# Optimization experiments

Hardware: AMD Instinct MI355X
Metric: run time of the kernel (lower is better)

Reference implementation:

```python
import jax, jax.numpy as jnp
import numpy as np

NUM_NODES = 100000
OUT_CHANNELS = 64
NUM_EDGES = 3200000


def setup_inputs() -> dict:
    key = jax.random.key(0)
    k1, k2, k3 = jax.random.split(key, 3)
    edge_index = jax.random.randint(k1, (2, NUM_EDGES), 0, NUM_NODES, dtype=jnp.int64) if jax.config.jax_enable_x64 else jax.random.randint(k1, (2, NUM_EDGES), 0, NUM_NODES, dtype=jnp.int32)
    # nn.Linear default init: U(-1/sqrt(fan_in), 1/sqrt(fan_in)); use randn-scale for a correctness baseline
    W_weight = jax.random.normal(k2, (OUT_CHANNELS, NUM_NODES), dtype=jnp.float32) * (1.0 / np.sqrt(NUM_NODES))
    W_bias = jax.random.normal(k3, (OUT_CHANNELS,), dtype=jnp.float32) * (1.0 / np.sqrt(NUM_NODES))
    return {"edge_index": edge_index, "W_weight": W_weight, "W_bias": W_bias}


def reference(edge_index, W_weight, W_bias):
    # A is the [N, N] binary COO adjacency (duplicate edges sum, matching
    # an uncoalesced torch sparse COO matmul). logits = A @ W_weight.T + b.
    num_nodes = W_weight.shape[1]
    row = edge_index[0] - jnp.min(edge_index[0])  # row = row - row.min()
    col = edge_index[1]
    Wt = W_weight.T  # [N, C]
    # SpMM as gather + segment-sum: logits[i] = sum_{(i,j) in E} Wt[j]
    logits = jax.ops.segment_sum(Wt[col], row, num_segments=num_nodes)  # [N, C]
    logits = logits + W_bias
    return jax.nn.log_softmax(logits, axis=1)
```

## Files before the change

kernel.cpp:

```cpp
#include <hip/hip_runtime.h>
#include <hip/hip_bf16.h>
#include <hip/hip_fp8.h>
#include <limits.h>

#define NUM_NODES 100000
#define OUT_CH 64
#define NUM_EDGES 3200000
#define BROWS 64
#define BSHIFT 6
#define NBUCK 1563
#define NBUCK_EXT 3125
#define NPBLK 128
#define EPB (NUM_EDGES / NPBLK)
#define I4PB (EPB / 4)
#define STAGECAP 4096
#define NTRANS 1563
#define FP8_SCALE 256.0f
#define FP8_INV (1.0f / 256.0f)

typedef float v2f __attribute__((ext_vector_type(2)));

__device__ __forceinline__ float fp8_decode_slow(unsigned b) {
    unsigned s = b >> 7, e = (b >> 3) & 0xF, m = b & 7;
    float v = (e == 0) ? ldexpf((float)m, -9) : ldexpf((float)(8 + m), (int)e - 10);
    return s ? -v : v;
}

__global__ __launch_bounds__(256) void LINK_62689342652831_mth_kernel(
    const float* __restrict__ W, unsigned char* __restrict__ Wt8,
    const int* __restrict__ rows, int* __restrict__ minp, int* __restrict__ hist2d) {
    __shared__ float tile[64][65];
    if (blockIdx.x < NTRANS) {
        int n0 = blockIdx.x * 64;
        int tx = threadIdx.x & 63;
        int ty = threadIdx.x >> 6;
        for (int c = ty; c < 64; c += 4) {
            int n = n0 + tx;
            tile[c][tx] = (n < NUM_NODES) ? W[(size_t)c * NUM_NODES + n] : 0.0f;
        }
        __syncthreads();
        for (int i = ty; i < 64; i += 4) {
            int n = n0 + i;
            if (n < NUM_NODES) {
                __hip_fp8_e4m3 q(FP8_SCALE * tile[tx][i]);
                Wt8[(size_t)n * OUT_CH + tx] = *reinterpret_cast<unsigned char*>(&q);
            }
        }
    } else {
        int blk = blockIdx.x - NTRANS;
        int* h = (int*)tile;
        int* sm = (int*)tile + 2048;
        for (int i = threadIdx.x; i < NBUCK; i += 256) h[i] = 0;
        __syncthreads();
        const int4* r4 = (const int4*)rows;
        int m = INT_MAX;
        for (int i = threadIdx.x; i < I4PB; i += 256) {
            int4 v = r4[blk * I4PB + i];
            m = min(m, min(min(v.x, v.y), min(v.z, v.w)));
            atomicAdd(&h[(unsigned)v.x >> BSHIFT], 1);
            atomicAdd(&h[(unsigned)v.y >> BSHIFT], 1);
            atomicAdd(&h[(unsigned)v.z >> BSHIFT], 1);
            atomicAdd(&h[(unsigned)v.w >> BSHIFT], 1);
        }
        for (int off = 32; off > 0; off >>= 1) m = min(m, __shfl_xor(m, off, 64));
        if ((threadIdx.x & 63) == 0) sm[threadIdx.x >> 6] = m;
        __syncthreads();
        for (int i = threadIdx.x; i < NBUCK; i += 256) hist2d[blk * NBUCK + i] = h[i];
        if (threadIdx.x == 0)
            atomicMin(minp, min(min(sm[0], sm[1]), min(sm[2], sm[3])));
    }
}

__global__ __launch_bounds__(512) void LINK_62689342652831_colscan_kernel(
    int* __restrict__ hist2d, int* __restrict__ totals) {
    int lane = threadIdx.x & 63;
    int wid = threadIdx.x >> 6;
    int b = blockIdx.x * 8 + wid;
    if (b >= NBUCK) return;
    int carry = 0;
    for (int rnd = 0; rnd < NPBLK / 64; ++rnd) {
        int blk = rnd * 64 + lane;
        int v = hist2d[blk * NBUCK + b];
        int x = v;
        for (int off = 1; off < 64; off <<= 1) {
            int y = __shfl_up(x, off, 64);
            if (lane >= off) x += y;
        }
        hist2d[blk * NBUCK + b] = x - v + carry;
        carry += __shfl(x, 63, 64);
    }
    if (lane == 0) totals[b] = carry;
}

__global__ __launch_bounds__(1024) void LINK_62689342652831_bscan_kernel(
    const int* __restrict__ totals, int* __restrict__ bstart) {
    __shared__ int ss[1024];
    int t = threadIdx.x;
    int i0 = 2 * t, i1 = 2 * t + 1;
    int v0 = (i0 < NBUCK) ? totals[i0] : 0;
    int v1 = (i1 < NBUCK) ? totals[i1] : 0;
    int p1 = v0 + v1;
    ss[t] = p1;
    __syncthreads();
    for (int off = 1; off < 1024; off <<= 1) {
        int x = (t >= off) ? ss[t - off] : 0;
        __syncthreads();
        ss[t] += x;
        __syncthreads();
    }
    int texcl = ss[t] - p1;
    if (i0 < NBUCK) bstart[i0] = texcl;
    if (i1 < NBUCK) bstart[i1] = texcl + v0;
    if (t == 1023) bstart[NBUCK] = ss[1023];
}

__global__ __launch_bounds__(512) void LINK_62689342652831_part_kernel(
    const int* __restrict__ rows, const int* __restrict__ cols,
    const int* __restrict__ hist2d, const int* __restrict__ bstart,
    unsigned int* __restrict__ packed) {
    __shared__ int offs_l[NBUCK];
    __shared__ int lcur[NBUCK];
    int blk = blockIdx.x;
    for (int i = threadIdx.x; i < NBUCK; i += 512) {
        offs_l[i] = bstart[i] + hist2d[blk * NBUCK + i];
        lcur[i] = 0;
    }
    __syncthreads();
    const int4* r4 = (const int4*)rows;
    const int4* c4 = (const int4*)cols;
    for (int i = threadIdx.x; i < I4PB; i += 512) {
        int4 rv = r4[blk * I4PB + i];
        int4 cv = c4[blk * I4PB + i];
#pragma unroll
        for (int k = 0; k < 4; ++k) {
            int r = (k == 0) ? rv.x : (k == 1) ? rv.y : (k == 2) ? rv.z : rv.w;
            int c = (k == 0) ? cv.x : (k == 1) ? cv.y : (k == 2) ? cv.z : cv.w;
            int b = (unsigned)r >> BSHIFT;
            int pos = offs_l[b] + atomicAdd(&lcur[b], 1);
            packed[pos] = ((unsigned)(r & (BROWS - 1)) << 17) | (unsigned)c;
        }
    }
}

__global__ __launch_bounds__(256) void LINK_62689342652831_spmm_kernel(
    const unsigned int* __restrict__ packed, const int* __restrict__ bstart,
    const unsigned char* __restrict__ Wt8, const float* __restrict__ bias,
    const int* __restrict__ minp, float* __restrict__ out) {
    __shared__ unsigned int sorted[STAGECAP];
    __shared__ int rhist[BROWS];
    __shared__ int rstart[BROWS + 1];
    __shared__ int rcur[BROWS];

    int lane = threadIdx.x & 63;
    int wid = threadIdx.x >> 6;
    int b = blockIdx.x;
    int minv = *minp;
    if (b * BROWS - minv >= NUM_NODES) return;
    int s = 0, e = 0;
    if (b < NBUCK) { s = bstart[b]; e = bstart[b + 1]; }
    int n = e - s;

    if (n <= STAGECAP) {
        int a4 = (4 - (s & 3)) & 3;
        if (a4 > n) a4 = n;
        int nb = (n - a4) >> 2;
        int tl = a4 + nb * 4;
        const uint4* p4 = (const uint4*)(packed + s + a4);

        if (threadIdx.x < BROWS) rhist[threadIdx.x] = 0;
        __syncthreads();
        if (threadIdx.x < a4) atomicAdd(&rhist[packed[s + threadIdx.x] >> 17], 1);
        for (int i = threadIdx.x; i < nb; i += 256) {
            uint4 u = p4[i];
            atomicAdd(&rhist[u.x >> 17], 1);
            atomicAdd(&rhist[u.y >> 17], 1);
            atomicAdd(&rhist[u.z >> 17], 1);
            atomicAdd(&rhist[u.w >> 17], 1);
        }
        if (tl + (int)threadIdx.x < n)
            atomicAdd(&rhist[packed[s + tl + threadIdx.x] >> 17], 1);
        __syncthreads();
        if (threadIdx.x < 64) {
            int c0 = rhist[lane];
            int x0 = c0;
            for (int off = 1; off < 64; off <<= 1) {
                int y0 = __shfl_up(x0, off, 64);
                if (lane >= off) x0 += y0;
            }
            rstart[lane] = x0 - c0;
            rcur[lane] = x0 - c0;
            if (lane == 63) rstart[64] = x0;
        }
        __syncthreads();
        if (threadIdx.x < a4) {
            unsigned int u = packed[s + threadIdx.x];
            sorted[atomicAdd(&rcur[u >> 17], 1)] = u;
        }
        for (int i = threadIdx.x; i < nb; i += 256) {
            uint4 u = p4[i];
            sorted[atomicAdd(&rcur[u.x >> 17], 1)] = u.x;
            sorted[atomicAdd(&rcur[u.y >> 17], 1)] = u.y;
            sorted[atomicAdd(&rcur[u.z >> 17], 1)] = u.z;
            sorted[atomicAdd(&rcur[u.w >> 17], 1)] = u.w;
        }
        if (tl + (int)threadIdx.x < n) {
            unsigned int u = packed[s + tl + threadIdx.x];
            sorted[atomicAdd(&rcur[u >> 17], 1)] = u;
        }
        __syncthreads();

        const unsigned int* Wt1 = (const unsigned int*)Wt8;
        int q = lane >> 4;
        int ql = lane & 15;
        float b0 = bias[4 * ql], b1 = bias[4 * ql + 1],
              b2 = bias[4 * ql + 2], b3 = bias[4 * ql + 3];

        for (int r = wid; r < BROWS; r += 4) {
            int gr = b * BROWS + r - minv;
            if (gr < 0 || gr >= NUM_NODES) continue;
            int s0 = rstart[r], e0 = rstart[r + 1];
            v2f a01 = {0.0f, 0.0f}, a23 = {0.0f, 0.0f};
            int i = s0 + q;
            for (; i + 4 < e0; i += 8) {
                unsigned int ua = sorted[i], ub = sorted[i + 4];
                unsigned int wa = Wt1[(size_t)((ua & 0x1FFFFu) << 4) + ql];
                unsigned int wb = Wt1[(size_t)((ub & 0x1FFFFu) << 4) + ql];
#if __has_builtin(__builtin_amdgcn_cvt_pk_f32_fp8)
                a01 += __builtin_amdgcn_cvt_pk_f32_fp8((int)wa, false);
                a23 += __builtin_amdgcn_cvt_pk_f32_fp8((int)wa, true);
                a01 += __builtin_amdgcn_cvt_pk_f32_fp8((int)wb, false);
                a23 += __builtin_amdgcn_cvt_pk_f32_fp8((int)wb, true);
#else
                a01.x += fp8_decode_slow(wa & 0xFF) + fp8_decode_slow(wb & 0xFF);
                a01.y += fp8_decode_slow((wa >> 8) & 0xFF) + fp8_decode_slow((wb >> 8) & 0xFF);
                a23.x += fp8_decode_slow((wa >> 16) & 0xFF) + fp8_decode_slow((wb >> 16) & 0xFF);
                a23.y += fp8_decode_slow(wa >> 24) + fp8_decode_slow(wb >> 24);
#endif
            }
            for (; i < e0; i += 4) {
                unsigned int w = Wt1[(size_t)((sorted[i] & 0x1FFFFu) << 4) + ql];
#if __has_builtin(__builtin_amdgcn_cvt_pk_f32_fp8)
                a01 += __builtin_amdgcn_cvt_pk_f32_fp8((int)w, false);
                a23 += __builtin_amdgcn_cvt_pk_f32_fp8((int)w, true);
#else
                a01.x += fp8_decode_slow(w & 0xFF);
                a01.y += fp8_decode_slow((w >> 8) & 0xFF);
                a23.x += fp8_decode_slow((w >> 16) & 0xFF);
                a23.y += fp8_decode_slow(w >> 24);
#endif
            }
            float a0 = a01.x, a1 = a01.y, a2 = a23.x, a3 = a23.y;
            a0 += __shfl_xor(a0, 32, 64); a1 += __shfl_xor(a1, 32, 64);
            a2 += __shfl_xor(a2, 32, 64); a3 += __shfl_xor(a3, 32, 64);
            a0 += __shfl_xor(a0, 16, 64); a1 += __shfl_xor(a1, 16, 64);
            a2 += __shfl_xor(a2, 16, 64); a3 += __shfl_xor(a3, 16, 64);

            float x0 = a0 * FP8_INV + b0, x1 = a1 * FP8_INV + b1;
            float x2 = a2 * FP8_INV + b2, x3 = a3 * FP8_INV + b3;
            float m = fmaxf(fmaxf(x0, x1), fmaxf(x2, x3));
            for (int off = 8; off > 0; off >>= 1) m = fmaxf(m, __shfl_xor(m, off, 64));
            float ssum = expf(x0 - m) + expf(x1 - m) + expf(x2 - m) + expf(x3 - m);
            for (int off = 8; off > 0; off >>= 1) ssum += __shfl_xor(ssum, off, 64);
            float l = m + logf(ssum);
            if (lane < 16) {
                float4 o = {x0 - l, x1 - l, x2 - l, x3 - l};
                *(float4*)&out[(size_t)gr * OUT_CH + 4 * ql] = o;
            }
        }
    } else {
        float* acc = (float*)sorted;
        for (int i = threadIdx.x; i < BROWS * OUT_CH; i += 256) acc[i] = 0.0f;
        __syncthreads();
        for (int i = s + wid; i < e; i += 4) {
            unsigned int u = packed[i];
            float v = fp8_decode_slow(Wt8[(size_t)(u & 0x1FFFF) * OUT_CH + lane]);
            atomicAdd(&acc[(u >> 17) * OUT_CH + lane], v);
        }
        __syncthreads();
        float bsv = bias[lane];
        for (int r = wid; r < BROWS; r += 4) {
            int gr = b * BROWS + r - minv;
            if (gr < 0 || gr >= NUM_NODES) continue;
            float x = acc[r * OUT_CH + lane] * FP8_INV + bsv;
            float m = x;
            for (int off = 32; off > 0; off >>= 1) m = fmaxf(m, __shfl_xor(m, off, 64));
            float ex = expf(x - m);
            float ssum = ex;
            for (int off = 32; off > 0; off >>= 1) ssum += __shfl_xor(ssum, off, 64);
            out[(size_t)gr * OUT_CH + lane] = x - m - logf(ssum);
        }
    }
}

__global__ void LINK_62689342652831_minf_kernel(const int* __restrict__ rows, int n,
                                                int* __restrict__ minp) {
    int tid = blockIdx.x * blockDim.x + threadIdx.x;
    int stride = gridDim.x * blockDim.x;
    int m = INT_MAX;
    for (int i = tid; i < n; i += stride) m = min(m, rows[i]);
    for (int off = 32; off > 0; off >>= 1) m = min(m, __shfl_xor(m, off, 64));
    if ((threadIdx.x & 63) == 0) atomicMin(minp, m);
}

__global__ void LINK_62689342652831_scatter_kernel(const int* __restrict__ rows,
                                                   const int* __restrict__ cols,
                                                   const float* __restrict__ W,
                                                   const int* __restrict__ minp,
                                                   float* __restrict__ out) {
    int lane = threadIdx.x & 63;
    int gw = (blockIdx.x * blockDim.x + threadIdx.x) >> 6;
    int nw = (gridDim.x * blockDim.x) >> 6;
    int minv = *minp;
    for (int e = gw; e < NUM_EDGES; e += nw) {
        int r = rows[e] - minv;
        int c = cols[e];
        float v = W[(size_t)lane * NUM_NODES + c];
        unsafeAtomicAdd(&out[(size_t)r * 64 + lane], v);
    }
}

__global__ void LINK_62689342652831_logsoftmax_kernel(float* __restrict__ out,
                                                      const float* __restrict__ bias) {
    int lane = threadIdx.x & 63;
    int gw = (blockIdx.x * blockDim.x + threadIdx.x) >> 6;
    int nw = (gridDim.x * blockDim.x) >> 6;
    float b = bias[lane];
    for (int r = gw; r < NUM_NODES; r += nw) {
        float x = out[(size_t)r * 64 + lane] + b;
        float m = x;
        for (int off = 32; off > 0; off >>= 1) m = fmaxf(m, __shfl_xor(m, off, 64));
        float e = expf(x - m);
        float s = e;
        for (int off = 32; off > 0; off >>= 1) s += __shfl_xor(s, off, 64);
        out[(size_t)r * 64 + lane] = x - m - logf(s);
    }
}

extern "C" void kernel_launch(void* const* d_in, const int* in_sizes, int n_in,
                              void* d_out, int out_size, void* d_ws, size_t ws_size,
                              hipStream_t stream) {
    const int* edges = (const int*)d_in[0];
    const int* rows = edges;
    const int* cols = edges + NUM_EDGES;
    const float* W = (const float*)d_in[1];
    const float* bias = (const float*)d_in[2];
    float* out = (float*)d_out;

    char* ws = (char*)d_ws;
    const size_t OFF_MIN = 0;
    const size_t OFF_TOT = 1024;
    const size_t OFF_BSTART = 16384;
    const size_t OFF_H2D = 32768;
    const size_t OFF_PACKED = 1024 * 1024;
    const size_t OFF_WT8 = OFF_PACKED + (size_t)NUM_EDGES * 4;
    const size_t need = OFF_WT8 + (size_t)NUM_NODES * OUT_CH;

    int* minp = (int*)(ws + OFF_MIN);
    int* totals = (int*)(ws + OFF_TOT);
    int* bstart = (int*)(ws + OFF_BSTART);
    int* hist2d = (int*)(ws + OFF_H2D);
    unsigned int* packed = (unsigned int*)(ws + OFF_PACKED);
    unsigned char* Wt8 = (unsigned char*)(ws + OFF_WT8);

    hipMemsetAsync(minp, 0x7f, sizeof(int), stream);

    if (ws_size >= need) {
        LINK_62689342652831_mth_kernel<<<NTRANS + NPBLK, 256, 0, stream>>>(W, Wt8, rows,
                                                                           minp, hist2d);
        LINK_62689342652831_colscan_kernel<<<(NBUCK + 7) / 8, 512, 0, stream>>>(hist2d, totals);
        LINK_62689342652831_bscan_kernel<<<1, 1024, 0, stream>>>(totals, bstart);
        LINK_62689342652831_part_kernel<<<NPBLK, 512, 0, stream>>>(rows, cols, hist2d,
                                                                   bstart, packed);
        LINK_62689342652831_spmm_kernel<<<NBUCK_EXT, 256, 0, stream>>>(packed, bstart, Wt8,
                                                                       bias, minp, out);
    } else {
        LINK_62689342652831_minf_kernel<<<2048, 256, 0, stream>>>(rows, NUM_EDGES, minp);
        hipMemsetAsync(d_out, 0, (size_t)out_size * sizeof(float), stream);
        LINK_62689342652831_scatter_kernel<<<2048, 256, 0, stream>>>(rows, cols, W, minp, out);
        LINK_62689342652831_logsoftmax_kernel<<<4096, 256, 0, stream>>>(out, bias);
    }
}
```

Measured before the change: 122.7 us.

## Fuse histogram and scan into partition kernel; gather per-block segments in SpMM

The separate histogram, column-scan and bucket-scan kernels are removed. Each partition block now builds its own local bucket histogram, scans it locally and scatters edges into its own slice of the packed array. The SpMM kernel reads the per-block segment offsets for its bucket, prefix-sums them and gathers edges from all 256 partition segments through a binary search into a shared staging buffer. This cuts two kernel launches and a global scan pass. In exchange the SpMM kernel does scattered, non-contiguous reads, a 256-way scan per block and more shared memory, and the transpose now runs serially before partitioning instead of alongside the histogram.

```diff
diff --git a/kernel.cpp b/kernel.cpp
--- a/kernel.cpp
+++ b/kernel.cpp
@@ -9,8 +9,9 @@
 #define BROWS 64
 #define BSHIFT 6
 #define NBUCK 1563
+#define NBUCKP (NBUCK + 1)
 #define NBUCK_EXT 3125
-#define NPBLK 128
+#define NPBLK 256
 #define EPB (NUM_EDGES / NPBLK)
 #define I4PB (EPB / 4)
 #define STAGECAP 4096
@@ -26,109 +27,89 @@
     return s ? -v : v;
 }
 
-__global__ __launch_bounds__(256) void LINK_62689342652831_mth_kernel(
-    const float* __restrict__ W, unsigned char* __restrict__ Wt8,
-    const int* __restrict__ rows, int* __restrict__ minp, int* __restrict__ hist2d) {
+__global__ __launch_bounds__(256) void LINK_62689342652831_transpose_kernel(
+    const float* __restrict__ W, unsigned char* __restrict__ Wt8) {
     __shared__ float tile[64][65];
-    if (blockIdx.x < NTRANS) {
-        int n0 = blockIdx.x * 64;
-        int tx = threadIdx.x & 63;
-        int ty = threadIdx.x >> 6;
-        for (int c = ty; c < 64; c += 4) {
-            int n = n0 + tx;
-            tile[c][tx] = (n < NUM_NODES) ? W[(size_t)c * NUM_NODES + n] : 0.0f;
-        }
-        __syncthreads();
-        for (int i = ty; i < 64; i += 4) {
-            int n = n0 + i;
-            if (n < NUM_NODES) {
-                __hip_fp8_e4m3 q(FP8_SCALE * tile[tx][i]);
-                Wt8[(size_t)n * OUT_CH + tx] = *reinterpret_cast<unsigned char*>(&q);
-            }
-        }
-    } else {
-        int blk = blockIdx.x - NTRANS;
-        int* h = (int*)tile;
-        int* sm = (int*)tile + 2048;
-        for (int i = threadIdx.x; i < NBUCK; i += 256) h[i] = 0;
-        __syncthreads();
-        const int4* r4 = (const int4*)rows;
-        int m = INT_MAX;
-        for (int i = threadIdx.x; i < I4PB; i += 256) {
-            int4 v = r4[blk * I4PB + i];
-            m = min(m, min(min(v.x, v.y), min(v.z, v.w)));
-            atomicAdd(&h[(unsigned)v.x >> BSHIFT], 1);
-            atomicAdd(&h[(unsigned)v.y >> BSHIFT], 1);
-            atomicAdd(&h[(unsigned)v.z >> BSHIFT], 1);
-            atomicAdd(&h[(unsigned)v.w >> BSHIFT], 1);
-        }
-        for (int off = 32; off > 0; off >>= 1) m = min(m, __shfl_xor(m, off, 64));
-        if ((threadIdx.x & 63) == 0) sm[threadIdx.x >> 6] = m;
-        __syncthreads();
-        for (int i = threadIdx.x; i < NBUCK; i += 256) hist2d[blk * NBUCK + i] = h[i];
-        if (threadIdx.x == 0)
-            atomicMin(minp, min(min(sm[0], sm[1]), min(sm[2], sm[3])));
-    }
-}
-
-__global__ __launch_bounds__(512) void LINK_62689342652831_colscan_kernel(
-    int* __restrict__ hist2d, int* __restrict__ totals) {
-    int lane = threadIdx.x & 63;
-    int wid = threadIdx.x >> 6;
-    int b = blockIdx.x * 8 + wid;
-    if (b >= NBUCK) return;
-    int carry = 0;
-    for (int rnd = 0; rnd < NPBLK / 64; ++rnd) {
-        int blk = rnd * 64 + lane;
-        int v = hist2d[blk * NBUCK + b];
-        int x = v;
-        for (int off = 1; off < 64; off <<= 1) {
-            int y = __shfl_up(x, off, 64);
-            if (lane >= off) x += y;
-        }
-        hist2d[blk * NBUCK + b] = x - v + carry;
-        carry += __shfl(x, 63, 64);
-    }
-    if (lane == 0) totals[b] = carry;
-}
-
-__global__ __launch_bounds__(1024) void LINK_62689342652831_bscan_kernel(
-    const int* __restrict__ totals, int* __restrict__ bstart) {
-    __shared__ int ss[1024];
-    int t = threadIdx.x;
-    int i0 = 2 * t, i1 = 2 * t + 1;
-    int v0 = (i0 < NBUCK) ? totals[i0] : 0;
-    int v1 = (i1 < NBUCK) ? totals[i1] : 0;
-    int p1 = v0 + v1;
-    ss[t] = p1;
-    __syncthreads();
-    for (int off = 1; off < 1024; off <<= 1) {
-        int x = (t >= off) ? ss[t - off] : 0;
-        __syncthreads();
-        ss[t] += x;
-        __syncthreads();
-    }
-    int texcl = ss[t] - p1;
-    if (i0 < NBUCK) bstart[i0] = texcl;
-    if (i1 < NBUCK) bstart[i1] = texcl + v0;
-    if (t == 1023) bstart[NBUCK] = ss[1023];
+    int n0 = blockIdx.x * 64;
+    int tx = threadIdx.x & 63;
+    int ty = threadIdx.x >> 6;
+    for (int c = ty; c < 64; c += 4) {
+        int n = n0 + tx;
+        tile[c][tx] = (n < NUM_NODES) ? W[(size_t)c * NUM_NODES + n] : 0.0f;
+    }
+    __syncthreads();
+    for (int i = ty; i < 64; i += 4) {
+        int n = n0 + i;
+        if (n < NUM_NODES) {
+            __hip_fp8_e4m3 q(FP8_SCALE * tile[tx][i]);
+            Wt8[(size_t)n * OUT_CH + tx] = *reinterpret_cast<unsigned char*>(&q);
+        }
+    }
 }
 
 __global__ __launch_bounds__(512) void LINK_62689342652831_part_kernel(
     const int* __restrict__ rows, const int* __restrict__ cols,
-    const int* __restrict__ hist2d, const int* __restrict__ bstart,
+    int* __restrict__ minp, int* __restrict__ loffT,
     unsigned int* __restrict__ packed) {
-    __shared__ int offs_l[NBUCK];
+    __shared__ int h[NBUCK];
     __shared__ int lcur[NBUCK];
+    __shared__ int ss[512];
+    __shared__ int sm8[8];
+    int tid = threadIdx.x;
     int blk = blockIdx.x;
-    for (int i = threadIdx.x; i < NBUCK; i += 512) {
-        offs_l[i] = bstart[i] + hist2d[blk * NBUCK + i];
-        lcur[i] = 0;
-    }
-    __syncthreads();
+    int lane = tid & 63;
+    int wid = tid >> 6;
+
+    for (int i = tid; i < NBUCK; i += 512) { h[i] = 0; lcur[i] = 0; }
+    __syncthreads();
+
     const int4* r4 = (const int4*)rows;
+    int m = INT_MAX;
+    for (int i = tid; i < I4PB; i += 512) {
+        int4 v = r4[blk * I4PB + i];
+        m = min(m, min(min(v.x, v.y), min(v.z, v.w)));
+        atomicAdd(&h[(unsigned)v.x >> BSHIFT], 1);
+        atomicAdd(&h[(unsigned)v.y >> BSHIFT], 1);
+        atomicAdd(&h[(unsigned)v.z >> BSHIFT], 1);
+        atomicAdd(&h[(unsigned)v.w >> BSHIFT], 1);
+    }
+    for (int off = 32; off > 0; off >>= 1) m = min(m, __shfl_xor(m, off, 64));
+    if (lane == 0) sm8[wid] = m;
+    __syncthreads();
+    if (tid == 0) {
+        int mm = sm8[0];
+#pragma unroll
+        for (int k = 1; k < 8; ++k) mm = min(mm, sm8[k]);
+        atomicMin(minp, mm);
+    }
+
+    int base = tid * 4;
+    int v0 = (base + 0 < NBUCK) ? h[base + 0] : 0;
+    int v1 = (base + 1 < NBUCK) ? h[base + 1] : 0;
+    int v2 = (base + 2 < NBUCK) ? h[base + 2] : 0;
+    int v3 = (base + 3 < NBUCK) ? h[base + 3] : 0;
+    int run = v0 + v1 + v2 + v3;
+    ss[tid] = run;
+    __syncthreads();
+    for (int off = 1; off < 512; off <<= 1) {
+        int x = (tid >= off) ? ss[tid - off] : 0;
+        __syncthreads();
+        ss[tid] += x;
+        __syncthreads();
+    }
+    int acc = ss[tid] - run;
+    if (base + 0 < NBUCK) { h[base + 0] = acc; loffT[blk * NBUCKP + base + 0] = acc; }
+    acc += v0;
+    if (base + 1 < NBUCK) { h[base + 1] = acc; loffT[blk * NBUCKP + base + 1] = acc; }
+    acc += v1;
+    if (base + 2 < NBUCK) { h[base + 2] = acc; loffT[blk * NBUCKP + base + 2] = acc; }
+    acc += v2;
+    if (base + 3 < NBUCK) { h[base + 3] = acc; loffT[blk * NBUCKP + base + 3] = acc; }
+    if (tid == 0) loffT[blk * NBUCKP + NBUCK] = EPB;
+    __syncthreads();
+
     const int4* c4 = (const int4*)cols;
-    for (int i = threadIdx.x; i < I4PB; i += 512) {
+    for (int i = tid; i < I4PB; i += 512) {
         int4 rv = r4[blk * I4PB + i];
         int4 cv = c4[blk * I4PB + i];
 #pragma unroll
@@ -136,51 +117,67 @@
             int r = (k == 0) ? rv.x : (k == 1) ? rv.y : (k == 2) ? rv.z : rv.w;
             int c = (k == 0) ? cv.x : (k == 1) ? cv.y : (k == 2) ? cv.z : cv.w;
             int b = (unsigned)r >> BSHIFT;
-            int pos = offs_l[b] + atomicAdd(&lcur[b], 1);
+            int pos = blk * EPB + h[b] + atomicAdd(&lcur[b], 1);
             packed[pos] = ((unsigned)(r & (BROWS - 1)) << 17) | (unsigned)c;
         }
     }
 }
 
 __global__ __launch_bounds__(256) void LINK_62689342652831_spmm_kernel(
-    const unsigned int* __restrict__ packed, const int* __restrict__ bstart,
+    const unsigned int* __restrict__ packed, const int* __restrict__ loffT,
     const unsigned char* __restrict__ Wt8, const float* __restrict__ bias,
     const int* __restrict__ minp, float* __restrict__ out) {
+    __shared__ unsigned int stage[STAGECAP];
     __shared__ unsigned int sorted[STAGECAP];
+    __shared__ int rlo[NPBLK];
+    __shared__ int epre[NPBLK + 1];
     __shared__ int rhist[BROWS];
     __shared__ int rstart[BROWS + 1];
     __shared__ int rcur[BROWS];
 
-    int lane = threadIdx.x & 63;
-    int wid = threadIdx.x >> 6;
+    int tid = threadIdx.x;
+    int lane = tid & 63;
+    int wid = tid >> 6;
     int b = blockIdx.x;
     int minv = *minp;
     if (b * BROWS - minv >= NUM_NODES) return;
-    int s = 0, e = 0;
-    if (b < NBUCK) { s = bstart[b]; e = bstart[b + 1]; }
-    int n = e - s;
+
+    int lo = 0, len = 0;
+    if (b < NBUCK) {
+        lo = loffT[tid * NBUCKP + b];
+        int hi = loffT[tid * NBUCKP + b + 1];
+        len = hi - lo;
+    }
+    rlo[tid] = lo;
+    epre[tid] = len;
+    __syncthreads();
+    for (int off = 1; off < 256; off <<= 1) {
+        int x = (tid >= off) ? epre[tid - off] : 0;
+        __syncthreads();
+        epre[tid] += x;
+        __syncthreads();
+    }
+    int n = epre[NPBLK - 1];
+    int incl = epre[tid];
+    __syncthreads();
+    epre[tid] = incl - len;
+    if (tid == 0) epre[NPBLK] = n;
+    __syncthreads();
 
     if (n <= STAGECAP) {
-        int a4 = (4 - (s & 3)) & 3;
-        if (a4 > n) a4 = n;
-        int nb = (n - a4) >> 2;
-        int tl = a4 + nb * 4;
-        const uint4* p4 = (const uint4*)(packed + s + a4);
-
-        if (threadIdx.x < BROWS) rhist[threadIdx.x] = 0;
-        __syncthreads();
-        if (threadIdx.x < a4) atomicAdd(&rhist[packed[s + threadIdx.x] >> 17], 1);
-        for (int i = threadIdx.x; i < nb; i += 256) {
-            uint4 u = p4[i];
-            atomicAdd(&rhist[u.x >> 17], 1);
-            atomicAdd(&rhist[u.y >> 17], 1);
-            atomicAdd(&rhist[u.z >> 17], 1);
-            atomicAdd(&rhist[u.w >> 17], 1);
-        }
-        if (tl + (int)threadIdx.x < n)
-            atomicAdd(&rhist[packed[s + tl + threadIdx.x] >> 17], 1);
-        __syncthreads();
-        if (threadIdx.x < 64) {
+        for (int i = tid; i < n; i += 256) {
+            int lo2 = 0, hi2 = NPBLK;
+            while (hi2 - lo2 > 1) {
+                int mid = (lo2 + hi2) >> 1;
+                if (epre[mid] <= i) lo2 = mid; else hi2 = mid;
+            }
+            stage[i] = packed[lo2 * EPB + rlo[lo2] + (i - epre[lo2])];
+        }
+        if (tid < BROWS) rhist[tid] = 0;
+        __syncthreads();
+        for (int i = tid; i < n; i += 256) atomicAdd(&rhist[stage[i] >> 17], 1);
+        __syncthreads();
+        if (tid < 64) {
             int c0 = rhist[lane];
             int x0 = c0;
             for (int off = 1; off < 64; off <<= 1) {
@@ -192,19 +189,8 @@
             if (lane == 63) rstart[64] = x0;
         }
         __syncthreads();
-        if (threadIdx.x < a4) {
-            unsigned int u = packed[s + threadIdx.x];
-            sorted[atomicAdd(&rcur[u >> 17], 1)] = u;
-        }
-        for (int i = threadIdx.x; i < nb; i += 256) {
-            uint4 u = p4[i];
-            sorted[atomicAdd(&rcur[u.x >> 17], 1)] = u.x;
-            sorted[atomicAdd(&rcur[u.y >> 17], 1)] = u.y;
-            sorted[atomicAdd(&rcur[u.z >> 17], 1)] = u.z;
-            sorted[atomicAdd(&rcur[u.w >> 17], 1)] = u.w;
-        }
-        if (tl + (int)threadIdx.x < n) {
-            unsigned int u = packed[s + tl + threadIdx.x];
+        for (int i = tid; i < n; i += 256) {
+            unsigned int u = stage[i];
             sorted[atomicAdd(&rcur[u >> 17], 1)] = u;
         }
         __syncthreads();
@@ -268,13 +254,17 @@
             }
         }
     } else {
-        float* acc = (float*)sorted;
-        for (int i = threadIdx.x; i < BROWS * OUT_CH; i += 256) acc[i] = 0.0f;
-        __syncthreads();
-        for (int i = s + wid; i < e; i += 4) {
-            unsigned int u = packed[i];
-            float v = fp8_decode_slow(Wt8[(size_t)(u & 0x1FFFF) * OUT_CH + lane]);
-            atomicAdd(&acc[(u >> 17) * OUT_CH + lane], v);
+        float* acc = (float*)stage;
+        for (int i = tid; i < BROWS * OUT_CH; i += 256) acc[i] = 0.0f;
+        __syncthreads();
+        for (int k = wid; k < NPBLK; k += 4) {
+            int klen = epre[k + 1] - epre[k];
+            int kbase = k * EPB + rlo[k];
+            for (int j = 0; j < klen; ++j) {
+                unsigned int u = packed[kbase + j];
+                float v = fp8_decode_slow(Wt8[(size_t)(u & 0x1FFFF) * OUT_CH + lane]);
+                atomicAdd(&acc[(u >> 17) * OUT_CH + lane], v);
+            }
         }
         __syncthreads();
         float bsv = bias[lane];
@@ -348,30 +338,23 @@
 
     char* ws = (char*)d_ws;
     const size_t OFF_MIN = 0;
-    const size_t OFF_TOT = 1024;
-    const size_t OFF_BSTART = 16384;
-    const size_t OFF_H2D = 32768;
-    const size_t OFF_PACKED = 1024 * 1024;
+    const size_t OFF_LOFF = 1024;
+    const size_t OFF_PACKED = 2 * 1024 * 1024;
     const size_t OFF_WT8 = OFF_PACKED + (size_t)NUM_EDGES * 4;
     const size_t need = OFF_WT8 + (size_t)NUM_NODES * OUT_CH;
 
     int* minp = (int*)(ws + OFF_MIN);
-    int* totals = (int*)(ws + OFF_TOT);
-    int* bstart = (int*)(ws + OFF_BSTART);
-    int* hist2d = (int*)(ws + OFF_H2D);
+    int* loffT = (int*)(ws + OFF_LOFF);
     unsigned int* packed = (unsigned int*)(ws + OFF_PACKED);
     unsigned char* Wt8 = (unsigned char*)(ws + OFF_WT8);
 
     hipMemsetAsync(minp, 0x7f, sizeof(int), stream);
 
     if (ws_size >= need) {
-        LINK_62689342652831_mth_kernel<<<NTRANS + NPBLK, 256, 0, stream>>>(W, Wt8, rows,
-                                                                           minp, hist2d);
-        LINK_62689342652831_colscan_kernel<<<(NBUCK + 7) / 8, 512, 0, stream>>>(hist2d, totals);
-        LINK_62689342652831_bscan_kernel<<<1, 1024, 0, stream>>>(totals, bstart);
-        LINK_62689342652831_part_kernel<<<NPBLK, 512, 0, stream>>>(rows, cols, hist2d,
-                                                                   bstart, packed);
-        LINK_62689342652831_spmm_kernel<<<NBUCK_EXT, 256, 0, stream>>>(packed, bstart, Wt8,
+        LINK_62689342652831_transpose_kernel<<<NTRANS, 256, 0, stream>>>(W, Wt8);
+        LINK_62689342652831_part_kernel<<<NPBLK, 512, 0, stream>>>(rows, cols, minp,
+                                                                   loffT, packed);
+        LINK_62689342652831_spmm_kernel<<<NBUCK_EXT, 256, 0, stream>>>(packed, loffT, Wt8,
                                                                        bias, minp, out);
     } else {
         LINK_62689342652831_minf_kernel<<<2048, 256, 0, stream>>>(rows, NUM_EDGES, minp);
```

After: 149.9 us. +22.1%, slower.
